# Kernel tuning notes

Hardware: AMD Instinct MI355X
Metric: run time of the kernel (lower is better)

## Reference

```python
import jax, jax.numpy as jnp
import numpy as np

D = 512; H = 8; L = 6; DFF = 2048; V = 32000
B = 2; S_SRC = 1024; S_TRG = 1024
PAD_ID = 0
DH = D // H

def posenc(S, d):
    pos = np.arange(S)[:, None].astype(np.float32)
    i = np.arange(0, d, 2)[None, :].astype(np.float32)
    ang = pos / (10000.0 ** (i / d))
    pe = np.zeros((S, d), np.float32)
    pe[:, 0::2] = np.sin(ang)
    pe[:, 1::2] = np.cos(ang)
    return jnp.asarray(pe)

def layernorm(x, s, b):
    m = jnp.mean(x, -1, keepdims=True)
    v = jnp.var(x, -1, keepdims=True)
    return (x - m) * jax.lax.rsqrt(v + 1e-5) * s + b

def split_heads(x):
    b, s, _ = x.shape
    return x.reshape(b, s, H, DH).transpose(0, 2, 1, 3)  # [B,H,S,DH]

def merge_heads(x):
    b, h, s, dh = x.shape
    return x.transpose(0, 2, 1, 3).reshape(b, s, h * dh)

def attn(q, k, v, mask):
    # q,k,v: [B,H,Sq,DH]/[B,H,Sk,DH]; mask True = blocked, broadcastable to [B,H,Sq,Sk]
    scores = jnp.einsum('bhqd,bhkd->bhqk', q, k) * (DH ** -0.5)
    scores = jnp.where(mask, -1e9, scores)
    p = jax.nn.softmax(scores, axis=-1)
    return merge_heads(jnp.einsum('bhqk,bhkd->bhqd', p, v))

def setup_inputs() -> dict:
    key = jax.random.key(0)
    ks = iter(jax.random.split(key, 64))
    g = lambda shape, s=0.02: (jax.random.normal(next(ks), shape, jnp.float32) * s)
    inp = {}
    inp['batch_src'] = jax.random.randint(next(ks), (B, S_SRC), 0, V, jnp.int32)
    inp['trg_teacher'] = jax.random.randint(next(ks), (B, S_TRG), 0, V, jnp.int32)
    inp['src_emb'] = g((V, D)); inp['trg_emb'] = g((V, D))
    inp['fc_w'] = g((D, V)); inp['fc_b'] = jnp.zeros((V,), jnp.float32)
    # encoder layer stacks [L, ...]
    inp['enc_wqkv'] = g((L, D, 3 * D)); inp['enc_wo'] = g((L, D, D))
    inp['enc_ln1s'] = jnp.ones((L, D)); inp['enc_ln1b'] = jnp.zeros((L, D))
    inp['enc_w1'] = g((L, D, DFF)); inp['enc_b1'] = jnp.zeros((L, DFF))
    inp['enc_w2'] = g((L, DFF, D)); inp['enc_b2'] = jnp.zeros((L, D))
    inp['enc_ln2s'] = jnp.ones((L, D)); inp['enc_ln2b'] = jnp.zeros((L, D))
    # decoder layer stacks
    inp['dec_wqkv'] = g((L, D, 3 * D)); inp['dec_wo'] = g((L, D, D))
    inp['dec_ln1s'] = jnp.ones((L, D)); inp['dec_ln1b'] = jnp.zeros((L, D))
    inp['dec_wq'] = g((L, D, D)); inp['dec_wkv'] = g((L, D, 2 * D))
    inp['dec_woc'] = g((L, D, D))
    inp['dec_ln2s'] = jnp.ones((L, D)); inp['dec_ln2b'] = jnp.zeros((L, D))
    inp['dec_w1'] = g((L, D, DFF)); inp['dec_b1'] = jnp.zeros((L, DFF))
    inp['dec_w2'] = g((L, DFF, D)); inp['dec_b2'] = jnp.zeros((L, D))
    inp['dec_ln3s'] = jnp.ones((L, D)); inp['dec_ln3b'] = jnp.zeros((L, D))
    return inp

def reference(batch_src, trg_teacher, src_emb, trg_emb, fc_w, fc_b,
              enc_wqkv, enc_wo, enc_ln1s, enc_ln1b, enc_w1, enc_b1, enc_w2, enc_b2, enc_ln2s, enc_ln2b,
              dec_wqkv, dec_wo, dec_ln1s, dec_ln1b, dec_wq, dec_wkv, dec_woc, dec_ln2s, dec_ln2b,
              dec_w1, dec_b1, dec_w2, dec_b2, dec_ln3s, dec_ln3b):
    enc_mask = (batch_src == PAD_ID)[:, None, None, :]             # [B,1,1,S_src]
    causal = jnp.triu(jnp.ones((S_TRG, S_TRG), bool), 1)[None, None]  # [1,1,S,S]

    # ---- encoder ----
    x = src_emb[batch_src] * (D ** 0.5) + posenc(S_SRC, D)

    def enc_layer(x, p):
        wqkv, wo, l1s, l1b, w1, b1, w2, b2, l2s, l2b = p
        q, k, v = jnp.split(x @ wqkv, 3, axis=-1)
        o = attn(split_heads(q), split_heads(k), split_heads(v), enc_mask) @ wo
        x = layernorm(x + o, l1s, l1b)
        h = jax.nn.relu(x @ w1 + b1) @ w2 + b2
        return layernorm(x + h, l2s, l2b), None

    enc_out, _ = jax.lax.scan(enc_layer, x,
        (enc_wqkv, enc_wo, enc_ln1s, enc_ln1b, enc_w1, enc_b1, enc_w2, enc_b2, enc_ln2s, enc_ln2b))

    # ---- decoder (teacher forcing) ----
    y = trg_emb[trg_teacher] * (D ** 0.5) + posenc(S_TRG, D)

    def dec_layer(y, p):
        (wqkv, wo, l1s, l1b, wq, wkv, woc, l2s, l2b, w1, b1, w2, b2, l3s, l3b) = p
        q, k, v = jnp.split(y @ wqkv, 3, axis=-1)
        o = attn(split_heads(q), split_heads(k), split_heads(v), causal) @ wo
        y = layernorm(y + o, l1s, l1b)
        qc = y @ wq
        kc, vc = jnp.split(enc_out @ wkv, 2, axis=-1)
        oc = attn(split_heads(qc), split_heads(kc), split_heads(vc), enc_mask) @ woc
        y = layernorm(y + oc, l2s, l2b)
        h = jax.nn.relu(y @ w1 + b1) @ w2 + b2
        return layernorm(y + h, l3s, l3b), None

    dec_out, _ = jax.lax.scan(dec_layer, y,
        (dec_wqkv, dec_wo, dec_ln1s, dec_ln1b, dec_wq, dec_wkv, dec_woc, dec_ln2s, dec_ln2b,
         dec_w1, dec_b1, dec_w2, dec_b2, dec_ln3s, dec_ln3b))

    logits = dec_out @ fc_w + fc_b  # [B, S_TRG, V]
    return logits
```

## Files before the change

### kernel.cpp

```cpp
#include <hip/hip_runtime.h>
#include <cmath>

#define Dm   512
#define Hn   8
#define Ln   6
#define DFFm 2048
#define Vm   32000
#define Bn   2
#define Sn   1024
#define DHm  64
#define Mrows (Bn*Sn)

typedef unsigned short ushort_t;
typedef __attribute__((ext_vector_type(8))) short          s16x8;
typedef __attribute__((ext_vector_type(8))) unsigned short u16x8;
typedef __attribute__((ext_vector_type(4))) float          f32x4;

__device__ __forceinline__ ushort_t f2bf(float x) {
    union { float f; unsigned u; } un; un.f = x;
    unsigned r = un.u + 0x7fffu + ((un.u >> 16) & 1u);
    return (ushort_t)(r >> 16);
}

template<int TR, int NW>
__device__ __forceinline__ void stage_tile(const ushort_t* __restrict__ src, int ld,
                                           ushort_t* lds, int k0, int w, int lane)
{
    constexpr int CH = TR / (8 * NW);
    #pragma unroll
    for (int c = 0; c < CH; ++c) {
        const int rb = (w * CH + c) * 8;
        const int r  = rb + (lane >> 3);
        const ushort_t* gp = src + (size_t)r * ld + k0
                           + (((lane & 7) ^ ((lane >> 3) & 7)) << 3);
        __builtin_amdgcn_global_load_lds(
            (const __attribute__((address_space(1))) void*)gp,
            (__attribute__((address_space(3))) void*)(lds + rb * 64),
            16, 0, 0);
    }
}

__device__ __forceinline__ s16x8 ldrd(const ushort_t* lds, int r, int st)
{
    return *(const s16x8*)&lds[r * 64 + ((st ^ (r & 7)) << 3)];
}

template<int TM, int TN, int NW, bool OBF, bool BIAS, bool RELU, bool VTOUT, bool SWZ>
__global__ __launch_bounds__(NW * 64) void gemm_bf(
    const ushort_t* __restrict__ A, const ushort_t* __restrict__ Bt,
    void* __restrict__ Cv, const float* __restrict__ bias,
    int K, int lda, int ldb, int ldc,
    long A_sb, long A_sh, long B_sb, long B_sh, long C_sb, long C_sh, int nh,
    ushort_t* __restrict__ VTp, int voff)
{
    constexpr int WC = NW / 2;
    constexpr int FI = TM / 32;
    constexpr int FJ = TN / (16 * WC);
    __shared__ __align__(16) ushort_t As[2][TM * 64];
    __shared__ __align__(16) ushort_t Bs[2][TN * 64];

    const int z = blockIdx.z, b = z / nh, h = z - b * nh;
    A  += (size_t)b * A_sb + (size_t)h * A_sh;
    Bt += (size_t)b * B_sb + (size_t)h * B_sh;

    int bx = blockIdx.x, by = blockIdx.y;
    if constexpr (SWZ) {
        const int ncol = gridDim.x, nrow = gridDim.y;
        const int total = ncol * nrow;
        const int flat = bx + by * ncol;
        const int per = total >> 3;
        const int g = (flat & 7) * per + (flat >> 3);
        bx = g / nrow;
        by = g - bx * nrow;
    }

    const int tid  = threadIdx.x;
    const int w    = tid >> 6, lane = tid & 63;
    const int m0   = by * TM, n0 = bx * TN;
    const int rw   = (w / WC) * (TM / 2);
    const int cn   = (w % WC) * (TN / WC);
    const int l15  = lane & 15, l4 = lane >> 4;

    const ushort_t* Ab = A + (size_t)m0 * lda;
    const ushort_t* Bb = Bt + (size_t)n0 * ldb;

    f32x4 acc[FI][FJ] = {};

    stage_tile<TM, NW>(Ab, lda, As[0], 0, w, lane);
    stage_tile<TN, NW>(Bb, ldb, Bs[0], 0, w, lane);
    __syncthreads();

    const int nk = K >> 6;
    for (int t = 0; t < nk; ++t) {
        const int cur = t & 1;
        if (t + 1 < nk) {
            stage_tile<TM, NW>(Ab, lda, As[cur ^ 1], (t + 1) << 6, w, lane);
            stage_tile<TN, NW>(Bb, ldb, Bs[cur ^ 1], (t + 1) << 6, w, lane);
        }
        #pragma unroll
        for (int ks = 0; ks < 2; ++ks) {
            const int st = ks * 4 + l4;
            s16x8 av[FI], bv[FJ];
            #pragma unroll
            for (int i = 0; i < FI; ++i) av[i] = ldrd(As[cur], rw + i * 16 + l15, st);
            #pragma unroll
            for (int j = 0; j < FJ; ++j) bv[j] = ldrd(Bs[cur], cn + j * 16 + l15, st);
            #pragma unroll
            for (int i = 0; i < FI; ++i)
                #pragma unroll
                for (int j = 0; j < FJ; ++j)
                    acc[i][j] = __builtin_amdgcn_mfma_f32_16x16x32_bf16(
                                    av[i], bv[j], acc[i][j], 0, 0, 0);
        }
        __syncthreads();
    }

    const int colb = n0 + cn + l15;
    const int rowb = m0 + rw + (l4 << 2);
    float bvv[FJ];
    #pragma unroll
    for (int j = 0; j < FJ; ++j) bvv[j] = BIAS ? bias[colb + j * 16] : 0.f;

    if constexpr (OBF) {
        ushort_t* C = (ushort_t*)Cv + (size_t)b * C_sb + (size_t)h * C_sh;
        #pragma unroll
        for (int i = 0; i < FI; ++i)
            #pragma unroll
            for (int r = 0; r < 4; ++r) {
                const int row = rowb + i * 16 + r;
                #pragma unroll
                for (int j = 0; j < FJ; ++j) {
                    float v = acc[i][j][r] + bvv[j];
                    if (RELU) v = fmaxf(v, 0.f);
                    const int col = colb + j * 16;
                    if (VTOUT && col >= voff) {
                        const int hc = (col - voff) >> 6, d = (col - voff) & 63;
                        const int zz = (row >> 10) * 8 + hc;
                        VTp[(size_t)zz * (64 * Sn) + (size_t)d * Sn + (row & (Sn - 1))] = f2bf(v);
                    } else {
                        C[(size_t)row * ldc + col] = f2bf(v);
                    }
                }
            }
    } else {
        float* C = (float*)Cv + (size_t)b * C_sb + (size_t)h * C_sh;
        #pragma unroll
        for (int i = 0; i < FI; ++i)
            #pragma unroll
            for (int r = 0; r < 4; ++r) {
                const size_t row = rowb + i * 16 + r;
                #pragma unroll
                for (int j = 0; j < FJ; ++j) {
                    float v = acc[i][j][r] + bvv[j];
                    if (RELU) v = fmaxf(v, 0.f);
                    C[row * ldc + colb + j * 16] = v;
                }
            }
    }
}

template<int MODE>
__global__ __launch_bounds__(256) void flash_attn(
    const ushort_t* __restrict__ Qp, const ushort_t* __restrict__ Kp,
    const ushort_t* __restrict__ VTp, ushort_t* __restrict__ AO,
    const int* __restrict__ tok, int ldq, int ldk)
{
    __shared__ __align__(16) ushort_t Ks[2][64 * 64];
    __shared__ __align__(16) ushort_t Vs[2][64 * 64];
    __shared__ __align__(16) ushort_t Ps[4][16 * 64];
    __shared__ float msk[Sn];

    const int z = blockIdx.y, b = z >> 3, h = z & 7;
    const int qb = blockIdx.x * 64;
    const int tid = threadIdx.x, w = tid >> 6, lane = tid & 63;
    const int l15 = lane & 15, l4 = lane >> 4;

    const ushort_t* Qbase = Qp + (size_t)b * Sn * ldq + h * 64;
    const ushort_t* Kbase = Kp + (size_t)b * Sn * ldk + h * 64;
    const ushort_t* Vbase = VTp + (size_t)z * 64 * Sn;
    ushort_t* Obase = AO + ((size_t)(b * Sn + qb)) * Dm + h * 64;

    if (MODE == 0) {
        const int* tb = tok + (size_t)b * Sn;
        for (int i = tid; i < Sn; i += 256) msk[i] = (tb[i] == 0) ? 1.f : 0.f;
    }

    const int qrow = qb + w * 16 + l15;
    s16x8 qv[2];
    qv[0] = *(const s16x8*)(Qbase + (size_t)qrow * ldq + l4 * 8);
    qv[1] = *(const s16x8*)(Qbase + (size_t)qrow * ldq + 32 + l4 * 8);

    f32x4 o[4] = {};
    float m[4], lsum[4];
    #pragma unroll
    for (int r = 0; r < 4; ++r) { m[r] = -1e30f; lsum[r] = 0.f; }

    const int nt = (MODE == 1) ? (qb / 64 + 1) : (Sn / 64);

    stage_tile<64, 4>(Kbase, ldk, Ks[0], 0, w, lane);
    stage_tile<64, 4>(Vbase, Sn, Vs[0], 0, w, lane);
    __syncthreads();

    for (int kt = 0; kt < nt; ++kt) {
        const int cur = kt & 1;
        if (kt + 1 < nt) {
            stage_tile<64, 4>(Kbase + (size_t)((kt + 1) * 64) * ldk, ldk, Ks[cur ^ 1], 0, w, lane);
            stage_tile<64, 4>(Vbase, Sn, Vs[cur ^ 1], (kt + 1) * 64, w, lane);
        }

        f32x4 s[4] = {};
        #pragma unroll
        for (int ks = 0; ks < 2; ++ks) {
            const int st = ks * 4 + l4;
            #pragma unroll
            for (int j = 0; j < 4; ++j) {
                s16x8 bv = ldrd(Ks[cur], j * 16 + l15, st);
                s[j] = __builtin_amdgcn_mfma_f32_16x16x32_bf16(qv[ks], bv, s[j], 0, 0, 0);
            }
        }

        #pragma unroll
        for (int j = 0; j < 4; ++j) {
            const int col = kt * 64 + j * 16 + l15;
            #pragma unroll
            for (int r = 0; r < 4; ++r) {
                float v = s[j][r] * 0.125f;
                if (MODE == 0) { if (msk[col] != 0.f) v = -1e9f; }
                else           { if (col > qb + w * 16 + l4 * 4 + r) v = -1e9f; }
                s[j][r] = v;
            }
        }

        float mt[4];
        #pragma unroll
        for (int r = 0; r < 4; ++r)
            mt[r] = fmaxf(fmaxf(s[0][r], s[1][r]), fmaxf(s[2][r], s[3][r]));
        #pragma unroll
        for (int mk = 1; mk < 16; mk <<= 1)
            #pragma unroll
            for (int r = 0; r < 4; ++r)
                mt[r] = fmaxf(mt[r], __shfl_xor(mt[r], mk));

        float al[4];
        #pragma unroll
        for (int r = 0; r < 4; ++r) {
            const float mn = fmaxf(m[r], mt[r]);
            al[r] = __expf(m[r] - mn);
            m[r] = mn;
        }

        float rs[4] = {0.f, 0.f, 0.f, 0.f};
        ushort_t* pw = Ps[w];
        #pragma unroll
        for (int j = 0; j < 4; ++j) {
            const int slot = j * 2 + (l15 >> 3), e = l15 & 7;
            #pragma unroll
            for (int r = 0; r < 4; ++r) {
                const float pvv = __expf(s[j][r] - m[r]);
                rs[r] += pvv;
                const int row = l4 * 4 + r;
                pw[row * 64 + ((slot ^ (row & 7)) << 3) + e] = f2bf(pvv);
            }
        }
        #pragma unroll
        for (int mk = 1; mk < 16; mk <<= 1)
            #pragma unroll
            for (int r = 0; r < 4; ++r)
                rs[r] += __shfl_xor(rs[r], mk);
        #pragma unroll
        for (int r = 0; r < 4; ++r) lsum[r] = lsum[r] * al[r] + rs[r];

        #pragma unroll
        for (int jd = 0; jd < 4; ++jd)
            #pragma unroll
            for (int r = 0; r < 4; ++r)
                o[jd][r] *= al[r];
        #pragma unroll
        for (int ks2 = 0; ks2 < 2; ++ks2) {
            const int st2 = ks2 * 4 + l4;
            s16x8 pa = ldrd(pw, l15, st2);
            #pragma unroll
            for (int jd = 0; jd < 4; ++jd) {
                s16x8 bv2 = ldrd(Vs[cur], jd * 16 + l15, st2);
                o[jd] = __builtin_amdgcn_mfma_f32_16x16x32_bf16(pa, bv2, o[jd], 0, 0, 0);
            }
        }
        __syncthreads();
    }

    #pragma unroll
    for (int r = 0; r < 4; ++r) lsum[r] = 1.f / lsum[r];
    #pragma unroll
    for (int jd = 0; jd < 4; ++jd)
        #pragma unroll
        for (int r = 0; r < 4; ++r)
            Obase[(size_t)(w * 16 + l4 * 4 + r) * Dm + jd * 16 + l15] =
                f2bf(o[jd][r] * lsum[r]);
}

struct WEnt { const float* src; ushort_t* dst; int R, C, tile0; };
struct WPack { WEnt e[12]; };

__global__ __launch_bounds__(256) void wcvt_all(WPack p)
{
    const int bid = blockIdx.x;
    int i = 0;
    #pragma unroll
    for (int k = 1; k < 12; ++k) if (bid >= p.e[k].tile0) i = k;
    const WEnt wd = p.e[i];
    const int rel = bid - wd.tile0;
    const int tC = wd.C >> 5, tR = wd.R >> 5;
    const int tpl = tC * tR;
    const int l = rel / tpl, t2 = rel - l * tpl;
    const int ty = t2 / tC, tx = t2 - ty * tC;

    const float* in  = wd.src + (size_t)l * wd.R * wd.C;
    ushort_t*    out = wd.dst + (size_t)l * wd.R * wd.C;

    __shared__ float tbuf[32][33];
    const int r0 = ty * 32, c0 = tx * 32;
    const int tid = threadIdx.x;
    const int r = tid >> 5, c = tid & 31;
    #pragma unroll
    for (int q = 0; q < 4; ++q)
        tbuf[r + q * 8][c] = in[(size_t)(r0 + r + q * 8) * wd.C + c0 + c];
    __syncthreads();
    const int c2 = tid >> 5, r2 = tid & 31;
    #pragma unroll
    for (int q = 0; q < 4; ++q)
        out[(size_t)(c0 + c2 + q * 8) * wd.R + r0 + r2] = f2bf(tbuf[r2][c2 + q * 8]);
}

__global__ __launch_bounds__(256) void add_ln(
    float* __restrict__ x, const float* __restrict__ o,
    const float* __restrict__ s, const float* __restrict__ bb,
    ushort_t* __restrict__ xbf)
{
    const long row = blockIdx.x;
    const int t = threadIdx.x;
    float* xr = x + row * Dm;
    const float* orr = o + row * Dm;
    float v0 = xr[t] + orr[t];
    float v1 = xr[t + 256] + orr[t + 256];

    float sum = v0 + v1, ssq = v0 * v0 + v1 * v1;
    __shared__ float red[8];
    for (int off = 32; off; off >>= 1) {
        sum += __shfl_down(sum, off);
        ssq += __shfl_down(ssq, off);
    }
    const int lane = t & 63, w = t >> 6;
    if (lane == 0) { red[w] = sum; red[4 + w] = ssq; }
    __syncthreads();
    sum = red[0] + red[1] + red[2] + red[3];
    ssq = red[4] + red[5] + red[6] + red[7];

    const float mean = sum * (1.f / Dm);
    const float var  = ssq * (1.f / Dm) - mean * mean;
    const float r = rsqrtf(var + 1e-5f);
    const float r0 = (v0 - mean) * r * s[t] + bb[t];
    const float r1 = (v1 - mean) * r * s[t + 256] + bb[t + 256];
    xr[t] = r0; xr[t + 256] = r1;
    xbf[row * Dm + t] = f2bf(r0);
    xbf[row * Dm + t + 256] = f2bf(r1);
}

__global__ __launch_bounds__(256) void embed_pe(
    const int* __restrict__ tokA, const float* __restrict__ embA,
    float* __restrict__ outA, ushort_t* __restrict__ outbfA,
    const int* __restrict__ tokB, const float* __restrict__ embB,
    float* __restrict__ outB, ushort_t* __restrict__ outbfB)
{
    const int bs = blockIdx.x;
    const int s = bs % Sn;
    const int t = threadIdx.x;
    const int*      tok   = blockIdx.y ? tokB : tokA;
    const float*    emb   = blockIdx.y ? embB : embA;
    float*          out   = blockIdx.y ? outB : outA;
    ushort_t*       outbf = blockIdx.y ? outbfB : outbfA;
    const int token = tok[bs];
    #pragma unroll
    for (int r = 0; r < 2; ++r) {
        const int d = t + r * 256;
        const int i = d & ~1;
        const float ang = (float)s * powf(10000.0f, -(float)i / (float)Dm);
        const float pe = (d & 1) ? cosf(ang) : sinf(ang);
        const float v = emb[(size_t)token * Dm + d] * 22.627416997969522f + pe;
        out[(size_t)bs * Dm + d] = v;
        outbf[(size_t)bs * Dm + d] = f2bf(v);
    }
}

extern "C" void kernel_launch(void* const* d_in, const int* in_sizes, int n_in,
                              void* d_out, int out_size, void* d_ws, size_t ws_size,
                              hipStream_t stream)
{
    const int*   batch_src = (const int*)d_in[0];
    const int*   trg       = (const int*)d_in[1];
    const float* src_emb   = (const float*)d_in[2];
    const float* trg_emb   = (const float*)d_in[3];
    const float* fc_w      = (const float*)d_in[4];
    const float* fc_b      = (const float*)d_in[5];
    const float* enc_wqkv  = (const float*)d_in[6];
    const float* enc_wo    = (const float*)d_in[7];
    const float* enc_ln1s  = (const float*)d_in[8];
    const float* enc_ln1b  = (const float*)d_in[9];
    const float* enc_w1    = (const float*)d_in[10];
    const float* enc_b1    = (const float*)d_in[11];
    const float* enc_w2    = (const float*)d_in[12];
    const float* enc_b2    = (const float*)d_in[13];
    const float* enc_ln2s  = (const float*)d_in[14];
    const float* enc_ln2b  = (const float*)d_in[15];
    const float* dec_wqkv  = (const float*)d_in[16];
    const float* dec_wo    = (const float*)d_in[17];
    const float* dec_ln1s  = (const float*)d_in[18];
    const float* dec_ln1b  = (const float*)d_in[19];
    const float* dec_wq    = (const float*)d_in[20];
    const float* dec_wkv   = (const float*)d_in[21];
    const float* dec_woc   = (const float*)d_in[22];
    const float* dec_ln2s  = (const float*)d_in[23];
    const float* dec_ln2b  = (const float*)d_in[24];
    const float* dec_w1    = (const float*)d_in[25];
    const float* dec_b1    = (const float*)d_in[26];
    const float* dec_w2    = (const float*)d_in[27];
    const float* dec_b2    = (const float*)d_in[28];
    const float* dec_ln3s  = (const float*)d_in[29];
    const float* dec_ln3b  = (const float*)d_in[30];
    (void)in_sizes; (void)n_in; (void)out_size; (void)ws_size;

    char* p = (char*)d_ws;
    auto alloc = [&](size_t bytes) { char* r = p; p += (bytes + 255) & ~(size_t)255; return r; };
    float*    X     = (float*)alloc((size_t)Mrows * Dm * 4);
    float*    Y     = (float*)alloc((size_t)Mrows * Dm * 4);
    float*    O     = (float*)alloc((size_t)Mrows * Dm * 4);
    ushort_t* Xbf   = (ushort_t*)alloc((size_t)Mrows * Dm * 2);
    ushort_t* Ybf   = (ushort_t*)alloc((size_t)Mrows * Dm * 2);
    ushort_t* QKVbf = (ushort_t*)alloc((size_t)Mrows * 3 * Dm * 2);
    ushort_t* AObf  = (ushort_t*)alloc((size_t)Mrows * Dm * 2);
    ushort_t* FHbf  = (ushort_t*)alloc((size_t)Mrows * DFFm * 2);
    ushort_t* QCbf  = (ushort_t*)alloc((size_t)Mrows * Dm * 2);
    ushort_t* KVbf  = (ushort_t*)alloc((size_t)Mrows * 2 * Dm * 2);
    ushort_t* VT    = (ushort_t*)alloc((size_t)16 * DHm * Sn * 2);
    ushort_t* ewqkv_t = (ushort_t*)alloc((size_t)Ln * 3 * Dm * Dm * 2);
    ushort_t* ewo_t   = (ushort_t*)alloc((size_t)Ln * Dm * Dm * 2);
    ushort_t* ew1_t   = (ushort_t*)alloc((size_t)Ln * DFFm * Dm * 2);
    ushort_t* ew2_t   = (ushort_t*)alloc((size_t)Ln * Dm * DFFm * 2);
    ushort_t* dwqkv_t = (ushort_t*)alloc((size_t)Ln * 3 * Dm * Dm * 2);
    ushort_t* dwo_t   = (ushort_t*)alloc((size_t)Ln * Dm * Dm * 2);
    ushort_t* dwq_t   = (ushort_t*)alloc((size_t)Ln * Dm * Dm * 2);
    ushort_t* dwkv_t  = (ushort_t*)alloc((size_t)Ln * 2 * Dm * Dm * 2);
    ushort_t* dwoc_t  = (ushort_t*)alloc((size_t)Ln * Dm * Dm * 2);
    ushort_t* dw1_t   = (ushort_t*)alloc((size_t)Ln * DFFm * Dm * 2);
    ushort_t* dw2_t   = (ushort_t*)alloc((size_t)Ln * Dm * DFFm * 2);
    ushort_t* fcw_t   = (ushort_t*)alloc((size_t)Vm * Dm * 2);

    {
        WPack pk;
        auto set = [&](int i, const float* s, ushort_t* d, int R, int C, int nl, int& acc) {
            pk.e[i] = { s, d, R, C, acc };
            acc += (R >> 5) * (C >> 5) * nl;
        };
        int acc = 0;
        set(0,  enc_wqkv, ewqkv_t, Dm,   3 * Dm, Ln, acc);
        set(1,  enc_wo,   ewo_t,   Dm,   Dm,     Ln, acc);
        set(2,  enc_w1,   ew1_t,   Dm,   DFFm,   Ln, acc);
        set(3,  enc_w2,   ew2_t,   DFFm, Dm,     Ln, acc);
        set(4,  dec_wqkv, dwqkv_t, Dm,   3 * Dm, Ln, acc);
        set(5,  dec_wo,   dwo_t,   Dm,   Dm,     Ln, acc);
        set(6,  dec_wq,   dwq_t,   Dm,   Dm,     Ln, acc);
        set(7,  dec_wkv,  dwkv_t,  Dm,   2 * Dm, Ln, acc);
        set(8,  dec_woc,  dwoc_t,  Dm,   Dm,     Ln, acc);
        set(9,  dec_w1,   dw1_t,   Dm,   DFFm,   Ln, acc);
        set(10, dec_w2,   dw2_t,   DFFm, Dm,     Ln, acc);
        set(11, fc_w,     fcw_t,   Dm,   Vm,     1,  acc);
        wcvt_all<<<acc, 256, 0, stream>>>(pk);
    }

    embed_pe<<<dim3(Mrows, 2), 256, 0, stream>>>(
        batch_src, src_emb, X, Xbf, trg, trg_emb, Y, Ybf);

    for (int l = 0; l < Ln; ++l) {
        gemm_bf<64,128,4,true,false,false,true,false><<<dim3(12, 32, 1), 256, 0, stream>>>(
            Xbf, ewqkv_t + (size_t)l * 3 * Dm * Dm, QKVbf, nullptr,
            Dm, Dm, Dm, 3 * Dm, 0,0,0,0,0,0, 1, VT, 2 * Dm);
        flash_attn<0><<<dim3(16, 16), 256, 0, stream>>>(
            QKVbf, QKVbf + Dm, VT, AObf, batch_src, 3 * Dm, 3 * Dm);
        gemm_bf<64,64,8,false,false,false,false,false><<<dim3(8, 32, 1), 512, 0, stream>>>(
            AObf, ewo_t + (size_t)l * Dm * Dm, O, nullptr,
            Dm, Dm, Dm, Dm, 0,0,0,0,0,0, 1, nullptr, 0);
        add_ln<<<Mrows, 256, 0, stream>>>(X, O, enc_ln1s + l * Dm, enc_ln1b + l * Dm, Xbf);
        gemm_bf<64,128,4,true,true,true,false,false><<<dim3(16, 32, 1), 256, 0, stream>>>(
            Xbf, ew1_t + (size_t)l * DFFm * Dm, FHbf, enc_b1 + l * DFFm,
            Dm, Dm, Dm, DFFm, 0,0,0,0,0,0, 1, nullptr, 0);
        gemm_bf<64,64,8,false,true,false,false,false><<<dim3(8, 32, 1), 512, 0, stream>>>(
            FHbf, ew2_t + (size_t)l * Dm * DFFm, O, enc_b2 + l * Dm,
            DFFm, DFFm, DFFm, Dm, 0,0,0,0,0,0, 1, nullptr, 0);
        add_ln<<<Mrows, 256, 0, stream>>>(X, O, enc_ln2s + l * Dm, enc_ln2b + l * Dm, Xbf);
    }

    for (int l = 0; l < Ln; ++l) {
        gemm_bf<64,128,4,true,false,false,true,false><<<dim3(12, 32, 1), 256, 0, stream>>>(
            Ybf, dwqkv_t + (size_t)l * 3 * Dm * Dm, QKVbf, nullptr,
            Dm, Dm, Dm, 3 * Dm, 0,0,0,0,0,0, 1, VT, 2 * Dm);
        flash_attn<1><<<dim3(16, 16), 256, 0, stream>>>(
            QKVbf, QKVbf + Dm, VT, AObf, nullptr, 3 * Dm, 3 * Dm);
        gemm_bf<64,64,8,false,false,false,false,false><<<dim3(8, 32, 1), 512, 0, stream>>>(
            AObf, dwo_t + (size_t)l * Dm * Dm, O, nullptr,
            Dm, Dm, Dm, Dm, 0,0,0,0,0,0, 1, nullptr, 0);
        add_ln<<<Mrows, 256, 0, stream>>>(Y, O, dec_ln1s + l * Dm, dec_ln1b + l * Dm, Ybf);

        gemm_bf<64,64,8,true,false,false,false,false><<<dim3(8, 32, 1), 512, 0, stream>>>(
            Ybf, dwq_t + (size_t)l * Dm * Dm, QCbf, nullptr,
            Dm, Dm, Dm, Dm, 0,0,0,0,0,0, 1, nullptr, 0);
        gemm_bf<64,128,4,true,false,false,true,false><<<dim3(8, 32, 1), 256, 0, stream>>>(
            Xbf, dwkv_t + (size_t)l * 2 * Dm * Dm, KVbf, nullptr,
            Dm, Dm, Dm, 2 * Dm, 0,0,0,0,0,0, 1, VT, Dm);
        flash_attn<0><<<dim3(16, 16), 256, 0, stream>>>(
            QCbf, KVbf, VT, AObf, batch_src, Dm, 2 * Dm);
        gemm_bf<64,64,8,false,false,false,false,false><<<dim3(8, 32, 1), 512, 0, stream>>>(
            AObf, dwoc_t + (size_t)l * Dm * Dm, O, nullptr,
            Dm, Dm, Dm, Dm, 0,0,0,0,0,0, 1, nullptr, 0);
        add_ln<<<Mrows, 256, 0, stream>>>(Y, O, dec_ln2s + l * Dm, dec_ln2b + l * Dm, Ybf);

        gemm_bf<64,128,4,true,true,true,false,false><<<dim3(16, 32, 1), 256, 0, stream>>>(
            Ybf, dw1_t + (size_t)l * DFFm * Dm, FHbf, dec_b1 + l * DFFm,
            Dm, Dm, Dm, DFFm, 0,0,0,0,0,0, 1, nullptr, 0);
        gemm_bf<64,64,8,false,true,false,false,false><<<dim3(8, 32, 1), 512, 0, stream>>>(
            FHbf, dw2_t + (size_t)l * Dm * DFFm, O, dec_b2 + l * Dm,
            DFFm, DFFm, DFFm, Dm, 0,0,0,0,0,0, 1, nullptr, 0);
        add_ln<<<Mrows, 256, 0, stream>>>(Y, O, dec_ln3s + l * Dm, dec_ln3b + l * Dm, Ybf);
    }

    gemm_bf<128,128,4,false,true,false,false,true><<<dim3(Vm / 128, 16, 1), 256, 0, stream>>>(
        Ybf, fcw_t, (float*)d_out, fc_b,
        Dm, Dm, Dm, Vm, 0,0,0,0,0,0, 1, nullptr, 0);
}
```

Baseline: 1.768 ms.

## Split flash attention KV loop across two warp groups with final merge

Flash attention blocks grow to 512 threads: two groups of four waves each handle alternating 64-key tiles for the same 64 query rows. Each group keeps its own double-buffered K/V tiles, and at the end the partial softmax states (o, m, lsum) are merged through shared memory. The aim is more parallelism for the small 256-block grid, cutting the serial KV loop length in half. In exchange it uses more shared memory per block and adds a merge step, which may lower occupancy.

```diff
diff --git a/kernel.cpp b/kernel.cpp
--- a/kernel.cpp
+++ b/kernel.cpp
@@ -160,19 +160,21 @@
 }
 
 template<int MODE>
-__global__ __launch_bounds__(256) void flash_attn(
+__global__ __launch_bounds__(512) void flash_attn(
     const ushort_t* __restrict__ Qp, const ushort_t* __restrict__ Kp,
     const ushort_t* __restrict__ VTp, ushort_t* __restrict__ AO,
     const int* __restrict__ tok, int ldq, int ldk)
 {
-    __shared__ __align__(16) ushort_t Ks[2][64 * 64];
-    __shared__ __align__(16) ushort_t Vs[2][64 * 64];
-    __shared__ __align__(16) ushort_t Ps[4][16 * 64];
+    __shared__ __align__(16) ushort_t Ks[2][2][64 * 64];
+    __shared__ __align__(16) ushort_t Vs[2][2][64 * 64];
+    __shared__ __align__(16) ushort_t Ps[8][16 * 64];
     __shared__ float msk[Sn];
+    __shared__ float mrg[4][64][25];
 
     const int z = blockIdx.y, b = z >> 3, h = z & 7;
     const int qb = blockIdx.x * 64;
     const int tid = threadIdx.x, w = tid >> 6, lane = tid & 63;
+    const int g = w >> 2, w4 = w & 3;
     const int l15 = lane & 15, l4 = lane >> 4;
 
     const ushort_t* Qbase = Qp + (size_t)b * Sn * ldq + h * 64;
@@ -182,10 +184,10 @@
 
     if (MODE == 0) {
         const int* tb = tok + (size_t)b * Sn;
-        for (int i = tid; i < Sn; i += 256) msk[i] = (tb[i] == 0) ? 1.f : 0.f;
-    }
-
-    const int qrow = qb + w * 16 + l15;
+        for (int i = tid; i < Sn; i += 512) msk[i] = (tb[i] == 0) ? 1.f : 0.f;
+    }
+
+    const int qrow = qb + w4 * 16 + l15;
     s16x8 qv[2];
     qv[0] = *(const s16x8*)(Qbase + (size_t)qrow * ldq + l4 * 8);
     qv[1] = *(const s16x8*)(Qbase + (size_t)qrow * ldq + 32 + l4 * 8);
@@ -196,106 +198,132 @@
     for (int r = 0; r < 4; ++r) { m[r] = -1e30f; lsum[r] = 0.f; }
 
     const int nt = (MODE == 1) ? (qb / 64 + 1) : (Sn / 64);
-
-    stage_tile<64, 4>(Kbase, ldk, Ks[0], 0, w, lane);
-    stage_tile<64, 4>(Vbase, Sn, Vs[0], 0, w, lane);
+    const int nIt = (nt + 1) >> 1;
+
+    if (g < nt) {
+        stage_tile<64, 4>(Kbase + (size_t)(g * 64) * ldk, ldk, Ks[g][0], 0, w4, lane);
+        stage_tile<64, 4>(Vbase, Sn, Vs[g][0], g * 64, w4, lane);
+    }
     __syncthreads();
 
-    for (int kt = 0; kt < nt; ++kt) {
-        const int cur = kt & 1;
-        if (kt + 1 < nt) {
-            stage_tile<64, 4>(Kbase + (size_t)((kt + 1) * 64) * ldk, ldk, Ks[cur ^ 1], 0, w, lane);
-            stage_tile<64, 4>(Vbase, Sn, Vs[cur ^ 1], (kt + 1) * 64, w, lane);
+    for (int it = 0; it < nIt; ++it) {
+        const int kt = 2 * it + g;
+        const int cur = it & 1;
+        if (kt + 2 < nt) {
+            stage_tile<64, 4>(Kbase + (size_t)((kt + 2) * 64) * ldk, ldk, Ks[g][cur ^ 1], 0, w4, lane);
+            stage_tile<64, 4>(Vbase, Sn, Vs[g][cur ^ 1], (kt + 2) * 64, w4, lane);
         }
-
-        f32x4 s[4] = {};
-        #pragma unroll
-        for (int ks = 0; ks < 2; ++ks) {
-            const int st = ks * 4 + l4;
+        if (kt < nt) {
+            f32x4 s[4] = {};
+            #pragma unroll
+            for (int ks = 0; ks < 2; ++ks) {
+                const int st = ks * 4 + l4;
+                #pragma unroll
+                for (int j = 0; j < 4; ++j) {
+                    s16x8 bv = ldrd(Ks[g][cur], j * 16 + l15, st);
+                    s[j] = __builtin_amdgcn_mfma_f32_16x16x32_bf16(qv[ks], bv, s[j], 0, 0, 0);
+                }
+            }
+
             #pragma unroll
             for (int j = 0; j < 4; ++j) {
-                s16x8 bv = ldrd(Ks[cur], j * 16 + l15, st);
-                s[j] = __builtin_amdgcn_mfma_f32_16x16x32_bf16(qv[ks], bv, s[j], 0, 0, 0);
-            }
-        }
-
-        #pragma unroll
-        for (int j = 0; j < 4; ++j) {
-            const int col = kt * 64 + j * 16 + l15;
+                const int col = kt * 64 + j * 16 + l15;
+                #pragma unroll
+                for (int r = 0; r < 4; ++r) {
+                    float v = s[j][r] * 0.125f;
+                    if (MODE == 0) { if (msk[col] != 0.f) v = -1e9f; }
+                    else           { if (col > qb + w4 * 16 + l4 * 4 + r) v = -1e9f; }
+                    s[j][r] = v;
+                }
+            }
+
+            float mt[4];
+            #pragma unroll
+            for (int r = 0; r < 4; ++r)
+                mt[r] = fmaxf(fmaxf(s[0][r], s[1][r]), fmaxf(s[2][r], s[3][r]));
+            #pragma unroll
+            for (int mk = 1; mk < 16; mk <<= 1)
+                #pragma unroll
+                for (int r = 0; r < 4; ++r)
+                    mt[r] = fmaxf(mt[r], __shfl_xor(mt[r], mk));
+
+            float al[4];
             #pragma unroll
             for (int r = 0; r < 4; ++r) {
-                float v = s[j][r] * 0.125f;
-                if (MODE == 0) { if (msk[col] != 0.f) v = -1e9f; }
-                else           { if (col > qb + w * 16 + l4 * 4 + r) v = -1e9f; }
-                s[j][r] = v;
-            }
-        }
-
-        float mt[4];
-        #pragma unroll
-        for (int r = 0; r < 4; ++r)
-            mt[r] = fmaxf(fmaxf(s[0][r], s[1][r]), fmaxf(s[2][r], s[3][r]));
-        #pragma unroll
-        for (int mk = 1; mk < 16; mk <<= 1)
-            #pragma unroll
-            for (int r = 0; r < 4; ++r)
-                mt[r] = fmaxf(mt[r], __shfl_xor(mt[r], mk));
-
-        float al[4];
-        #pragma unroll
-        for (int r = 0; r < 4; ++r) {
-            const float mn = fmaxf(m[r], mt[r]);
-            al[r] = __expf(m[r] - mn);
-            m[r] = mn;
-        }
-
-        float rs[4] = {0.f, 0.f, 0.f, 0.f};
-        ushort_t* pw = Ps[w];
-        #pragma unroll
-        for (int j = 0; j < 4; ++j) {
-            const int slot = j * 2 + (l15 >> 3), e = l15 & 7;
-            #pragma unroll
-            for (int r = 0; r < 4; ++r) {
-                const float pvv = __expf(s[j][r] - m[r]);
-                rs[r] += pvv;
-                const int row = l4 * 4 + r;
-                pw[row * 64 + ((slot ^ (row & 7)) << 3) + e] = f2bf(pvv);
-            }
-        }
-        #pragma unroll
-        for (int mk = 1; mk < 16; mk <<= 1)
-            #pragma unroll
-            for (int r = 0; r < 4; ++r)
-                rs[r] += __shfl_xor(rs[r], mk);
-        #pragma unroll
-        for (int r = 0; r < 4; ++r) lsum[r] = lsum[r] * al[r] + rs[r];
-
-        #pragma unroll
-        for (int jd = 0; jd < 4; ++jd)
-            #pragma unroll
-            for (int r = 0; r < 4; ++r)
-                o[jd][r] *= al[r];
-        #pragma unroll
-        for (int ks2 = 0; ks2 < 2; ++ks2) {
-            const int st2 = ks2 * 4 + l4;
-            s16x8 pa = ldrd(pw, l15, st2);
-            #pragma unroll
-            for (int jd = 0; jd < 4; ++jd) {
-                s16x8 bv2 = ldrd(Vs[cur], jd * 16 + l15, st2);
-                o[jd] = __builtin_amdgcn_mfma_f32_16x16x32_bf16(pa, bv2, o[jd], 0, 0, 0);
+                const float mn = fmaxf(m[r], mt[r]);
+                al[r] = __expf(m[r] - mn);
+                m[r] = mn;
+            }
+
+            float rs[4] = {0.f, 0.f, 0.f, 0.f};
+            ushort_t* pw = Ps[w];
+            #pragma unroll
+            for (int j = 0; j < 4; ++j) {
+                const int slot = j * 2 + (l15 >> 3), e = l15 & 7;
+                #pragma unroll
+                for (int r = 0; r < 4; ++r) {
+                    const float pvv = __expf(s[j][r] - m[r]);
+                    rs[r] += pvv;
+                    const int row = l4 * 4 + r;
+                    pw[row * 64 + ((slot ^ (row & 7)) << 3) + e] = f2bf(pvv);
+                }
+            }
+            #pragma unroll
+            for (int mk = 1; mk < 16; mk <<= 1)
+                #pragma unroll
+                for (int r = 0; r < 4; ++r)
+                    rs[r] += __shfl_xor(rs[r], mk);
+            #pragma unroll
+            for (int r = 0; r < 4; ++r) lsum[r] = lsum[r] * al[r] + rs[r];
+
+            #pragma unroll
+            for (int jd = 0; jd < 4; ++jd)
+                #pragma unroll
+                for (int r = 0; r < 4; ++r)
+                    o[jd][r] *= al[r];
+            #pragma unroll
+            for (int ks2 = 0; ks2 < 2; ++ks2) {
+                const int st2 = ks2 * 4 + l4;
+                s16x8 pa = ldrd(pw, l15, st2);
+                #pragma unroll
+                for (int jd = 0; jd < 4; ++jd) {
+                    s16x8 bv2 = ldrd(Vs[g][cur], jd * 16 + l15, st2);
+                    o[jd] = __builtin_amdgcn_mfma_f32_16x16x32_bf16(pa, bv2, o[jd], 0, 0, 0);
+                }
             }
         }
         __syncthreads();
     }
 
-    #pragma unroll
-    for (int r = 0; r < 4; ++r) lsum[r] = 1.f / lsum[r];
-    #pragma unroll
-    for (int jd = 0; jd < 4; ++jd)
-        #pragma unroll
-        for (int r = 0; r < 4; ++r)
-            Obase[(size_t)(w * 16 + l4 * 4 + r) * Dm + jd * 16 + l15] =
-                f2bf(o[jd][r] * lsum[r]);
+    if (g == 1) {
+        float* mp = mrg[w4][lane];
+        #pragma unroll
+        for (int jd = 0; jd < 4; ++jd)
+            #pragma unroll
+            for (int r = 0; r < 4; ++r)
+                mp[jd * 4 + r] = o[jd][r];
+        #pragma unroll
+        for (int r = 0; r < 4; ++r) { mp[16 + r] = m[r]; mp[20 + r] = lsum[r]; }
+    }
+    __syncthreads();
+    if (g == 0) {
+        const float* mp = mrg[w4][lane];
+        float a0[4], a1[4], inv[4];
+        #pragma unroll
+        for (int r = 0; r < 4; ++r) {
+            const float m1 = mp[16 + r];
+            const float mm = fmaxf(m[r], m1);
+            a0[r] = __expf(m[r] - mm);
+            a1[r] = __expf(m1 - mm);
+            inv[r] = 1.f / (lsum[r] * a0[r] + mp[20 + r] * a1[r]);
+        }
+        #pragma unroll
+        for (int jd = 0; jd < 4; ++jd)
+            #pragma unroll
+            for (int r = 0; r < 4; ++r)
+                Obase[(size_t)(w4 * 16 + l4 * 4 + r) * Dm + jd * 16 + l15] =
+                    f2bf((o[jd][r] * a0[r] + mp[jd * 4 + r] * a1[r]) * inv[r]);
+    }
 }
 
 struct WEnt { const float* src; ushort_t* dst; int R, C, tile0; };
@@ -483,7 +511,7 @@
         gemm_bf<64,128,4,true,false,false,true,false><<<dim3(12, 32, 1), 256, 0, stream>>>(
             Xbf, ewqkv_t + (size_t)l * 3 * Dm * Dm, QKVbf, nullptr,
             Dm, Dm, Dm, 3 * Dm, 0,0,0,0,0,0, 1, VT, 2 * Dm);
-        flash_attn<0><<<dim3(16, 16), 256, 0, stream>>>(
+        flash_attn<0><<<dim3(16, 16), 512, 0, stream>>>(
             QKVbf, QKVbf + Dm, VT, AObf, batch_src, 3 * Dm, 3 * Dm);
         gemm_bf<64,64,8,false,false,false,false,false><<<dim3(8, 32, 1), 512, 0, stream>>>(
             AObf, ewo_t + (size_t)l * Dm * Dm, O, nullptr,
@@ -502,7 +530,7 @@
         gemm_bf<64,128,4,true,false,false,true,false><<<dim3(12, 32, 1), 256, 0, stream>>>(
             Ybf, dwqkv_t + (size_t)l * 3 * Dm * Dm, QKVbf, nullptr,
             Dm, Dm, Dm, 3 * Dm, 0,0,0,0,0,0, 1, VT, 2 * Dm);
-        flash_attn<1><<<dim3(16, 16), 256, 0, stream>>>(
+        flash_attn<1><<<dim3(16, 16), 512, 0, stream>>>(
             QKVbf, QKVbf + Dm, VT, AObf, nullptr, 3 * Dm, 3 * Dm);
         gemm_bf<64,64,8,false,false,false,false,false><<<dim3(8, 32, 1), 512, 0, stream>>>(
             AObf, dwo_t + (size_t)l * Dm * Dm, O, nullptr,
@@ -515,7 +543,7 @@
         gemm_bf<64,128,4,true,false,false,true,false><<<dim3(8, 32, 1), 256, 0, stream>>>(
             Xbf, dwkv_t + (size_t)l * 2 * Dm * Dm, KVbf, nullptr,
             Dm, Dm, Dm, 2 * Dm, 0,0,0,0,0,0, 1, VT, Dm);
-        flash_attn<0><<<dim3(16, 16), 256, 0, stream>>>(
+        flash_attn<0><<<dim3(16, 16), 512, 0, stream>>>(
             QCbf, KVbf, VT, AObf, batch_src, Dm, 2 * Dm);
         gemm_bf<64,64,8,false,false,false,false,false><<<dim3(8, 32, 1), 512, 0, stream>>>(
             AObf, dwoc_t + (size_t)l * Dm * Dm, O, nullptr,
```

Measured after the change: 1.589 ms. 1.11x faster.
